# Kernel optimization log

Hardware: AMD Instinct MI355X
Metric: run time of the kernel (lower is better)

## Reference

```python
import jax, jax.numpy as jnp
import numpy as np

N_NODES = 50000
N_EDGES = 800000
NEG_SLOPE = 0.2


def _gat_layer(x, src, dst, W, al, ar, n_nodes):
    """Single multi-head GAT conv (DGL-style). Returns [N, H, D]."""
    H, D = al.shape
    feat = (x @ W).reshape(n_nodes, H, D)              # [N,H,D]
    el = jnp.einsum('nhd,hd->nh', feat, al)            # [N,H]
    er = jnp.einsum('nhd,hd->nh', feat, ar)            # [N,H]
    e = jax.nn.leaky_relu(el[src] + er[dst], NEG_SLOPE)  # [E,H]
    # numerically-stable edge softmax over incoming edges per dst node
    emax = jax.ops.segment_max(e, dst, num_segments=n_nodes)  # [N,H]
    emax = jnp.where(jnp.isfinite(emax), emax, 0.0)
    ee = jnp.exp(e - emax[dst])                        # [E,H]
    denom = jax.ops.segment_sum(ee, dst, num_segments=n_nodes)  # [N,H]
    alpha = ee / (denom[dst] + 1e-9)                   # [E,H]
    msg = alpha[:, :, None] * feat[src]                # [E,H,D]
    return jax.ops.segment_sum(msg, dst, num_segments=n_nodes)  # [N,H,D]


def setup_inputs() -> dict:
    key = jax.random.key(0)
    ks = jax.random.split(key, 9)
    features = jax.random.normal(ks[0], (N_NODES, 512), jnp.float32)
    src = jax.random.randint(ks[1], (N_EDGES,), 0, N_NODES)
    dst = jax.random.randint(ks[2], (N_EDGES,), 0, N_NODES)
    W1 = jax.random.normal(ks[3], (512, 256), jnp.float32) * 0.05
    al1 = jax.random.normal(ks[4], (8, 32), jnp.float32) * 0.05
    ar1 = jax.random.normal(ks[5], (8, 32), jnp.float32) * 0.05
    W2 = jax.random.normal(ks[6], (256, 320), jnp.float32) * 0.05
    al2 = jax.random.normal(ks[7], (8, 40), jnp.float32) * 0.05
    ar2 = jax.random.normal(ks[8], (8, 40), jnp.float32) * 0.05
    return {"features": features, "src": src, "dst": dst,
            "W1": W1, "al1": al1, "ar1": ar1,
            "W2": W2, "al2": al2, "ar2": ar2}


def reference(features, src, dst, W1, al1, ar1, W2, al2, ar2):
    n = features.shape[0]
    h = _gat_layer(features, src, dst, W1, al1, ar1, n)   # [N,8,32]
    h = jax.nn.elu(h.reshape(n, -1))                      # flatten(1) + ELU -> [N,256]
    h = _gat_layer(h, src, dst, W2, al2, ar2, n)          # [N,8,40]
    return h.mean(axis=1)                                 # head mean -> [N,40]
```

## Files before the change

### kernel.cpp

```cpp
#include <hip/hip_runtime.h>
#include <math.h>

typedef float f32x4 __attribute__((ext_vector_type(4)));
typedef __bf16 bf16x2 __attribute__((ext_vector_type(2)));
typedef __bf16 bf16x4 __attribute__((ext_vector_type(4)));
typedef __bf16 bf16x8 __attribute__((ext_vector_type(8)));


__global__ void hist_kernel(const int* __restrict__ dst, int* __restrict__ cnt, int E) {
    int e = blockIdx.x * blockDim.x + threadIdx.x;
    if (e < E) atomicAdd(&cnt[dst[e]], 1);
}

__global__ __launch_bounds__(256) void scan_blk(const int* __restrict__ cnt,
                                                int* __restrict__ incl,
                                                int* __restrict__ bsum, int n) {
    __shared__ int sd[256];
    const int t = threadIdx.x;
    int i = blockIdx.x * 256 + t;
    int v = (i < n) ? cnt[i] : 0;
    sd[t] = v;
    __syncthreads();
#pragma unroll
    for (int off = 1; off < 256; off <<= 1) {
        int x = (t >= off) ? sd[t - off] : 0;
        __syncthreads();
        sd[t] += x;
        __syncthreads();
    }
    if (i < n) incl[i] = sd[t];
    if (t == 255) bsum[blockIdx.x] = sd[255];
}

__global__ __launch_bounds__(256) void scan_top(const int* __restrict__ bsum,
                                                int* __restrict__ boff, int nb) {
    __shared__ int sd[256];
    const int t = threadIdx.x;
    int v = (t < nb) ? bsum[t] : 0;
    sd[t] = v;
    __syncthreads();
#pragma unroll
    for (int off = 1; off < 256; off <<= 1) {
        int x = (t >= off) ? sd[t - off] : 0;
        __syncthreads();
        sd[t] += x;
        __syncthreads();
    }
    if (t < nb) boff[t] = sd[t] - v;
}

__global__ void scan_fix(const int* __restrict__ incl, const int* __restrict__ boff,
                         const int* __restrict__ cnt, int* __restrict__ row_ptr,
                         int* __restrict__ cursor, int n) {
    int i = blockIdx.x * blockDim.x + threadIdx.x;
    if (i >= n) return;
    int total = incl[i] + boff[i >> 8];
    row_ptr[i + 1] = total;
    cursor[i] = total - cnt[i];
    if (i == 0) row_ptr[0] = 0;
}

__global__ void fill_kernel(const int* __restrict__ src, const int* __restrict__ dst,
                            int* __restrict__ cursor, int* __restrict__ ssrc,
                            int* __restrict__ sdst, int E) {
    int e = blockIdx.x * blockDim.x + threadIdx.x;
    if (e < E) {
        int d = dst[e];
        int pos = atomicAdd(&cursor[d], 1);
        ssrc[pos] = src[e];
        sdst[pos] = d;
    }
}

__global__ void pack_b_kernel(const float* __restrict__ W, __bf16* __restrict__ Bh,
                              __bf16* __restrict__ Bl, int K, int N) {
    int idx = blockIdx.x * blockDim.x + threadIdx.x;
    if (idx >= K * N) return;
    int e = idx & 7;
    int l = (idx >> 3) & 63;
    int c = idx >> 9;
    int ng = N >> 4;
    int g = c % ng;
    int k0 = (c / ng) << 5;
    int col = g * 16 + (l & 15);
    int k = k0 + ((l >> 4) << 3) + e;
    float x = W[(size_t)k * N + col];
    __bf16 h = (__bf16)x;
    Bh[idx] = h;
    Bl[idx] = (__bf16)(x - (float)h);
}

template <int BN, int NREP, bool FP32A>
__global__ __launch_bounds__(128) void gemm_fused(
    const float* __restrict__ Af, const __bf16* __restrict__ Ahg,
    const __bf16* __restrict__ Alg, const __bf16* __restrict__ Bph,
    const __bf16* __restrict__ Bpl, const float* __restrict__ al,
    const float* __restrict__ ar, __bf16* __restrict__ featb,
    float* __restrict__ el, float* __restrict__ er, int M, int K) {
    constexpr int WN = NREP * 16;
    constexpr int D = BN / 8;

    __shared__ __align__(16) __bf16 Ah[2][32][40];
    __shared__ __align__(16) __bf16 Al[2][32][40];
    __shared__ __align__(16) float ctile[2][16][WN + 1];

    const int t = threadIdx.x;
    const int lane = t & 63;
    const int wid = t >> 6;
    const int row0 = blockIdx.x * 32;
    const int colw = wid * WN;
    const int fr = lane & 15;
    const int kq = lane >> 4;
    const int kg = kq * 8;
    const int sr = t >> 2;
    const int sc = (t & 3) * 8;

    float4 av0, av1;
    bf16x8 avh, avl;

    auto loadA = [&](int k0) {
        int gr = row0 + sr;
        if (gr >= M) gr = M - 1;
        if constexpr (FP32A) {
            av0 = *(const float4*)&Af[(size_t)gr * K + k0 + sc];
            av1 = *(const float4*)&Af[(size_t)gr * K + k0 + sc + 4];
        } else {
            avh = *(const bf16x8*)&Ahg[(size_t)gr * K + k0 + sc];
            avl = *(const bf16x8*)&Alg[(size_t)gr * K + k0 + sc];
        }
    };
    auto storeA = [&](int p) {
        if constexpr (FP32A) {
            __bf16 h0 = (__bf16)av0.x, h1 = (__bf16)av0.y, h2 = (__bf16)av0.z,
                   h3 = (__bf16)av0.w;
            __bf16 h4 = (__bf16)av1.x, h5 = (__bf16)av1.y, h6 = (__bf16)av1.z,
                   h7 = (__bf16)av1.w;
            bf16x8 hv = {h0, h1, h2, h3, h4, h5, h6, h7};
            bf16x8 lv = {(__bf16)(av0.x - (float)h0), (__bf16)(av0.y - (float)h1),
                         (__bf16)(av0.z - (float)h2), (__bf16)(av0.w - (float)h3),
                         (__bf16)(av1.x - (float)h4), (__bf16)(av1.y - (float)h5),
                         (__bf16)(av1.z - (float)h6), (__bf16)(av1.w - (float)h7)};
            *(bf16x8*)&Ah[p][sr][sc] = hv;
            *(bf16x8*)&Al[p][sr][sc] = lv;
        } else {
            *(bf16x8*)&Ah[p][sr][sc] = avh;
            *(bf16x8*)&Al[p][sr][sc] = avl;
        }
    };

    f32x4 acc[2][NREP] = {};

    loadA(0);
    int p = 0;
    for (int k0 = 0; k0 < K; k0 += 32) {
        storeA(p);
        if (k0 + 32 < K) loadA(k0 + 32);
        bf16x8 bh[NREP], bl[NREP];
        const int c0 = (k0 >> 5) * (BN >> 4) + (colw >> 4);
#pragma unroll
        for (int n = 0; n < NREP; ++n) {
            size_t o = (size_t)(c0 + n) * 512 + lane * 8;
            bh[n] = *(const bf16x8*)&Bph[o];
            bl[n] = *(const bf16x8*)&Bpl[o];
        }
        __syncthreads();
        bf16x8 ah0 = *(const bf16x8*)&Ah[p][fr][kg];
        bf16x8 ah1 = *(const bf16x8*)&Ah[p][fr + 16][kg];
        bf16x8 al0 = *(const bf16x8*)&Al[p][fr][kg];
        bf16x8 al1 = *(const bf16x8*)&Al[p][fr + 16][kg];
#pragma unroll
        for (int n = 0; n < NREP; ++n) {
            acc[0][n] = __builtin_amdgcn_mfma_f32_16x16x32_bf16(ah0, bh[n], acc[0][n], 0, 0, 0);
            acc[0][n] = __builtin_amdgcn_mfma_f32_16x16x32_bf16(al0, bh[n], acc[0][n], 0, 0, 0);
            acc[0][n] = __builtin_amdgcn_mfma_f32_16x16x32_bf16(ah0, bl[n], acc[0][n], 0, 0, 0);
            acc[1][n] = __builtin_amdgcn_mfma_f32_16x16x32_bf16(ah1, bh[n], acc[1][n], 0, 0, 0);
            acc[1][n] = __builtin_amdgcn_mfma_f32_16x16x32_bf16(al1, bh[n], acc[1][n], 0, 0, 0);
            acc[1][n] = __builtin_amdgcn_mfma_f32_16x16x32_bf16(ah1, bl[n], acc[1][n], 0, 0, 0);
        }
        p ^= 1;
    }

#pragma unroll
    for (int m = 0; m < 2; ++m) {
        int rbase = row0 + m * 16 + kq * 4;
#pragma unroll
        for (int n = 0; n < NREP; ++n) {
            int col = colw + n * 16 + fr;
#pragma unroll
            for (int i = 0; i < 4; ++i) {
                int r = rbase + i;
                if (r < M) featb[(size_t)r * BN + col] = (__bf16)acc[m][n][i];
            }
        }
    }

#pragma unroll
    for (int m = 0; m < 2; ++m) {
#pragma unroll
        for (int n = 0; n < NREP; ++n)
#pragma unroll
            for (int i = 0; i < 4; ++i)
                ctile[wid][kq * 4 + i][n * 16 + fr] = acc[m][n][i];
        int r = lane & 15;
        int hh = lane >> 4;
        int h = wid * 4 + hh;
        float sl = 0.f, sr_ = 0.f;
#pragma unroll 8
        for (int d = 0; d < D; ++d) {
            float v = ctile[wid][r][hh * D + d];
            sl += v * al[h * D + d];
            sr_ += v * ar[h * D + d];
        }
        int gr = row0 + m * 16 + r;
        if (gr < M) {
            el[(size_t)gr * 8 + h] = sl;
            er[(size_t)gr * 8 + h] = sr_;
        }
        __syncthreads();
    }
}

__device__ __forceinline__ float leaky02(float x) { return x > 0.f ? x : 0.2f * x; }

__global__ void edge_score_kernel(const int* __restrict__ ssrc, const int* __restrict__ sdst,
                                  const float* __restrict__ el, const float* __restrict__ er,
                                  float* __restrict__ pe, int E) {
    int pos = blockIdx.x * blockDim.x + threadIdx.x;
    if (pos >= E) return;
    int s = ssrc[pos], d = sdst[pos];
    float4 l0 = *(const float4*)&el[(size_t)s * 8];
    float4 l1 = *(const float4*)&el[(size_t)s * 8 + 4];
    float4 r0 = *(const float4*)&er[(size_t)d * 8];
    float4 r1 = *(const float4*)&er[(size_t)d * 8 + 4];
    float4 o0 = {leaky02(l0.x + r0.x), leaky02(l0.y + r0.y),
                 leaky02(l0.z + r0.z), leaky02(l0.w + r0.w)};
    float4 o1 = {leaky02(l1.x + r1.x), leaky02(l1.y + r1.y),
                 leaky02(l1.z + r1.z), leaky02(l1.w + r1.w)};
    *(float4*)&pe[(size_t)pos * 8] = o0;
    *(float4*)&pe[(size_t)pos * 8 + 4] = o1;
}

template <int D, int MODE>
__global__ __launch_bounds__(256) void gat_aggregate(
    const __bf16* __restrict__ featb, const float* __restrict__ pe,
    const int* __restrict__ row_ptr, const int* __restrict__ ssrc,
    __bf16* __restrict__ outh, __bf16* __restrict__ outl,
    float* __restrict__ outf, int N) {
    constexpr int HD = 8 * D;
    constexpr int TAIL = HD - 256;
    __shared__ float red[4][MODE ? HD : 1];

    const int wid = threadIdx.x >> 6;
    const int lane = threadIdx.x & 63;
    const int n = blockIdx.x * 4 + wid;
    if (n >= N) return;

    const int beg = row_ptr[n];
    const int end = row_ptr[n + 1];
    const int hl = lane & 7;
    const int sl = lane >> 3;

    float m_l = -INFINITY;
    for (int idx = beg + sl; idx < end; idx += 8)
        m_l = fmaxf(m_l, pe[(size_t)idx * 8 + hl]);
    m_l = fmaxf(m_l, __shfl_xor(m_l, 8));
    m_l = fmaxf(m_l, __shfl_xor(m_l, 16));
    m_l = fmaxf(m_l, __shfl_xor(m_l, 32));
    float s_l = 0.f;
    for (int idx = beg + sl; idx < end; idx += 8)
        s_l += __expf(pe[(size_t)idx * 8 + hl] - m_l);
    s_l += __shfl_xor(s_l, 8);
    s_l += __shfl_xor(s_l, 16);
    s_l += __shfl_xor(s_l, 32);
    const float si_l = 1.0f / (s_l + 1e-9f);

    int hg[2], ht = 0;
#pragma unroll
    for (int g = 0; g < 2; ++g) hg[g] = (128 * g + 2 * lane) / D;
    if (TAIL) ht = (256 + lane) / D;

    float acc[2][2] = {};
    float acct = 0.f;
    int idx = beg;
    for (; idx + 4 <= end; idx += 4) {
        int ss[4];
        float aa[4];
#pragma unroll
        for (int uu = 0; uu < 4; ++uu) ss[uu] = ssrc[idx + uu];
#pragma unroll
        for (int uu = 0; uu < 4; ++uu)
            aa[uu] = __expf(pe[(size_t)(idx + uu) * 8 + hl] - m_l) * si_l;
        bf16x2 p[4][2];
        __bf16 pt[4];
#pragma unroll
        for (int uu = 0; uu < 4; ++uu) {
            const __bf16* f = featb + (size_t)ss[uu] * HD;
            p[uu][0] = *(const bf16x2*)&f[2 * lane];
            p[uu][1] = *(const bf16x2*)&f[128 + 2 * lane];
            if (TAIL) pt[uu] = f[256 + lane];
        }
#pragma unroll
        for (int uu = 0; uu < 4; ++uu) {
            float w0 = __shfl(aa[uu], hg[0]);
            float w1 = __shfl(aa[uu], hg[1]);
            acc[0][0] += w0 * (float)p[uu][0].x;
            acc[0][1] += w0 * (float)p[uu][0].y;
            acc[1][0] += w1 * (float)p[uu][1].x;
            acc[1][1] += w1 * (float)p[uu][1].y;
            if (TAIL) {
                float wt = __shfl(aa[uu], ht);
                acct += wt * (float)pt[uu];
            }
        }
    }
    for (; idx < end; ++idx) {
        int s = ssrc[idx];
        float a = __expf(pe[(size_t)idx * 8 + hl] - m_l) * si_l;
        const __bf16* f = featb + (size_t)s * HD;
        float w0 = __shfl(a, hg[0]);
        float w1 = __shfl(a, hg[1]);
        bf16x2 p0 = *(const bf16x2*)&f[2 * lane];
        bf16x2 p1 = *(const bf16x2*)&f[128 + 2 * lane];
        acc[0][0] += w0 * (float)p0.x;
        acc[0][1] += w0 * (float)p0.y;
        acc[1][0] += w1 * (float)p1.x;
        acc[1][1] += w1 * (float)p1.y;
        if (TAIL) {
            float wt = __shfl(a, ht);
            acct += wt * (float)f[256 + lane];
        }
    }

    if (MODE == 0) {
#pragma unroll
        for (int g = 0; g < 2; ++g) {
            float x0 = acc[g][0], x1 = acc[g][1];
            x0 = x0 > 0.f ? x0 : expm1f(x0);
            x1 = x1 > 0.f ? x1 : expm1f(x1);
            __bf16 h0 = (__bf16)x0, h1 = (__bf16)x1;
            bf16x2 vh = {h0, h1};
            bf16x2 vl = {(__bf16)(x0 - (float)h0), (__bf16)(x1 - (float)h1)};
            *(bf16x2*)&outh[(size_t)n * 256 + 128 * g + 2 * lane] = vh;
            *(bf16x2*)&outl[(size_t)n * 256 + 128 * g + 2 * lane] = vl;
        }
    } else {
#pragma unroll
        for (int g = 0; g < 2; ++g) {
            red[wid][128 * g + 2 * lane] = acc[g][0];
            red[wid][128 * g + 2 * lane + 1] = acc[g][1];
        }
        red[wid][256 + lane] = acct;
        if (lane < D) {
            float s = 0.f;
#pragma unroll
            for (int hh = 0; hh < 8; ++hh) s += red[wid][hh * D + lane];
            outf[(size_t)n * D + lane] = s * 0.125f;
        }
    }
}


extern "C" void kernel_launch(void* const* d_in, const int* in_sizes, int n_in,
                              void* d_out, int out_size, void* d_ws, size_t ws_size,
                              hipStream_t stream) {
    const float* features = (const float*)d_in[0];
    const int* src = (const int*)d_in[1];
    const int* dst = (const int*)d_in[2];
    const float* W1 = (const float*)d_in[3];
    const float* al1 = (const float*)d_in[4];
    const float* ar1 = (const float*)d_in[5];
    const float* W2 = (const float*)d_in[6];
    const float* al2 = (const float*)d_in[7];
    const float* ar2 = (const float*)d_in[8];

    const int N = in_sizes[0] / 512;
    const int E = in_sizes[1];

    char* ws = (char*)d_ws;
    size_t off = 0;
    auto alloc = [&](size_t bytes) -> void* {
        void* p = ws + off;
        off = (off + bytes + 255) & ~(size_t)255;
        return p;
    };
    __bf16* feat1b = (__bf16*)alloc((size_t)N * 256 * 2);
    __bf16* h_hi = (__bf16*)alloc((size_t)N * 256 * 2);
    __bf16* h_lo = (__bf16*)alloc((size_t)N * 256 * 2);
    __bf16* feat2b = (__bf16*)alloc((size_t)N * 320 * 2);
    float* pe = (float*)alloc((size_t)E * 8 * 4);
    float* el1 = (float*)alloc((size_t)N * 8 * 4);
    float* er1 = (float*)alloc((size_t)N * 8 * 4);
    float* el2 = (float*)alloc((size_t)N * 8 * 4);
    float* er2 = (float*)alloc((size_t)N * 8 * 4);
    int* cnt = (int*)alloc((size_t)N * 4);
    int* incl = (int*)alloc((size_t)N * 4);
    int* row_ptr = (int*)alloc((size_t)(N + 1) * 4);
    int* cursor = (int*)alloc((size_t)N * 4);
    int* bsum = (int*)alloc(256 * 4);
    int* boff = (int*)alloc(256 * 4);
    int* ssrc = (int*)alloc((size_t)E * 4);
    int* sdst = (int*)alloc((size_t)E * 4);
    __bf16* Bp1h = (__bf16*)alloc((size_t)512 * 256 * 2);
    __bf16* Bp1l = (__bf16*)alloc((size_t)512 * 256 * 2);
    __bf16* Bp2h = (__bf16*)alloc((size_t)256 * 320 * 2);
    __bf16* Bp2l = (__bf16*)alloc((size_t)256 * 320 * 2);

    const int NB = (N + 255) / 256;

    hipMemsetAsync(cnt, 0, (size_t)N * 4, stream);
    hist_kernel<<<(E + 255) / 256, 256, 0, stream>>>(dst, cnt, E);
    scan_blk<<<NB, 256, 0, stream>>>(cnt, incl, bsum, N);
    scan_top<<<1, 256, 0, stream>>>(bsum, boff, NB);
    scan_fix<<<NB, 256, 0, stream>>>(incl, boff, cnt, row_ptr, cursor, N);
    fill_kernel<<<(E + 255) / 256, 256, 0, stream>>>(src, dst, cursor, ssrc, sdst, E);

    pack_b_kernel<<<(512 * 256 + 255) / 256, 256, 0, stream>>>(W1, Bp1h, Bp1l, 512, 256);
    pack_b_kernel<<<(256 * 320 + 255) / 256, 256, 0, stream>>>(W2, Bp2h, Bp2l, 256, 320);

    const int mblk = (N + 31) / 32;

    gemm_fused<256, 8, true><<<mblk, 128, 0, stream>>>(
        features, nullptr, nullptr, Bp1h, Bp1l, al1, ar1, feat1b, el1, er1, N, 512);
    edge_score_kernel<<<(E + 255) / 256, 256, 0, stream>>>(ssrc, sdst, el1, er1, pe, E);
    gat_aggregate<32, 0><<<(N + 3) / 4, 256, 0, stream>>>(
        feat1b, pe, row_ptr, ssrc, h_hi, h_lo, nullptr, N);

    gemm_fused<320, 10, false><<<mblk, 128, 0, stream>>>(
        nullptr, h_hi, h_lo, Bp2h, Bp2l, al2, ar2, feat2b, el2, er2, N, 256);
    edge_score_kernel<<<(E + 255) / 256, 256, 0, stream>>>(ssrc, sdst, el2, er2, pe, E);
    gat_aggregate<40, 1><<<(N + 3) / 4, 256, 0, stream>>>(
        feat2b, pe, row_ptr, ssrc, nullptr, nullptr, (float*)d_out, N);
}
```

Measured before the change: 377.5 us.

## Use four waves per GEMM block with swizzled LDS A-tiles and union scratch

The fused GEMM now runs 256 threads (four waves) per block. Each wave covers half as many output columns, so it holds half as many accumulator and B registers, and launch bounds request higher occupancy. The A tile is stored in LDS in an MFMA-fragment-ready layout with an XOR swizzle, and it shares storage through a union with the epilogue ctile. The B global loads are now issued before the A store. The goal is more concurrent waves to hide global latency and fewer LDS bank conflicts. The cost is that each A load is now narrower (4 elements per thread), an extra barrier is added, and half the lanes sit idle in the el/er epilogue.

```diff
diff --git a/kernel.cpp b/kernel.cpp
--- a/kernel.cpp
+++ b/kernel.cpp
@@ -90,8 +90,10 @@
     Bl[idx] = (__bf16)(x - (float)h);
 }
 
+__device__ __forceinline__ int swz6(int x) { return x ^ (x >> 3); }
+
 template <int BN, int NREP, bool FP32A>
-__global__ __launch_bounds__(128) void gemm_fused(
+__global__ __launch_bounds__(256, 4) void gemm_fused(
     const float* __restrict__ Af, const __bf16* __restrict__ Ahg,
     const __bf16* __restrict__ Alg, const __bf16* __restrict__ Bph,
     const __bf16* __restrict__ Bpl, const float* __restrict__ al,
@@ -100,9 +102,15 @@
     constexpr int WN = NREP * 16;
     constexpr int D = BN / 8;
 
-    __shared__ __align__(16) __bf16 Ah[2][32][40];
-    __shared__ __align__(16) __bf16 Al[2][32][40];
-    __shared__ __align__(16) float ctile[2][16][WN + 1];
+    struct StageT {
+        __bf16 Ah[2][2][64][8];
+        __bf16 Al[2][2][64][8];
+    };
+    union Smem {
+        StageT s;
+        float ctile[4][16][WN + 1];
+    };
+    __shared__ __align__(16) Smem u;
 
     const int t = threadIdx.x;
     const int lane = t & 63;
@@ -111,40 +119,37 @@
     const int colw = wid * WN;
     const int fr = lane & 15;
     const int kq = lane >> 4;
-    const int kg = kq * 8;
-    const int sr = t >> 2;
-    const int sc = (t & 3) * 8;
-
-    float4 av0, av1;
-    bf16x8 avh, avl;
+    const int sr = t >> 3;
+    const int kc = (t & 7) * 4;
+    const int m_s = sr >> 4;
+    const int xs = (sr & 15) + 16 * (kc >> 3);
+    const int e0 = kc & 7;
+
+    float4 av;
+    bf16x4 avh, avl;
 
     auto loadA = [&](int k0) {
         int gr = row0 + sr;
         if (gr >= M) gr = M - 1;
         if constexpr (FP32A) {
-            av0 = *(const float4*)&Af[(size_t)gr * K + k0 + sc];
-            av1 = *(const float4*)&Af[(size_t)gr * K + k0 + sc + 4];
+            av = *(const float4*)&Af[(size_t)gr * K + k0 + kc];
         } else {
-            avh = *(const bf16x8*)&Ahg[(size_t)gr * K + k0 + sc];
-            avl = *(const bf16x8*)&Alg[(size_t)gr * K + k0 + sc];
+            avh = *(const bf16x4*)&Ahg[(size_t)gr * K + k0 + kc];
+            avl = *(const bf16x4*)&Alg[(size_t)gr * K + k0 + kc];
         }
     };
     auto storeA = [&](int p) {
         if constexpr (FP32A) {
-            __bf16 h0 = (__bf16)av0.x, h1 = (__bf16)av0.y, h2 = (__bf16)av0.z,
-                   h3 = (__bf16)av0.w;
-            __bf16 h4 = (__bf16)av1.x, h5 = (__bf16)av1.y, h6 = (__bf16)av1.z,
-                   h7 = (__bf16)av1.w;
-            bf16x8 hv = {h0, h1, h2, h3, h4, h5, h6, h7};
-            bf16x8 lv = {(__bf16)(av0.x - (float)h0), (__bf16)(av0.y - (float)h1),
-                         (__bf16)(av0.z - (float)h2), (__bf16)(av0.w - (float)h3),
-                         (__bf16)(av1.x - (float)h4), (__bf16)(av1.y - (float)h5),
-                         (__bf16)(av1.z - (float)h6), (__bf16)(av1.w - (float)h7)};
-            *(bf16x8*)&Ah[p][sr][sc] = hv;
-            *(bf16x8*)&Al[p][sr][sc] = lv;
+            __bf16 h0 = (__bf16)av.x, h1 = (__bf16)av.y, h2 = (__bf16)av.z,
+                   h3 = (__bf16)av.w;
+            bf16x4 hv = {h0, h1, h2, h3};
+            bf16x4 lv = {(__bf16)(av.x - (float)h0), (__bf16)(av.y - (float)h1),
+                         (__bf16)(av.z - (float)h2), (__bf16)(av.w - (float)h3)};
+            *(bf16x4*)&u.s.Ah[p][m_s][swz6(xs)][e0] = hv;
+            *(bf16x4*)&u.s.Al[p][m_s][swz6(xs)][e0] = lv;
         } else {
-            *(bf16x8*)&Ah[p][sr][sc] = avh;
-            *(bf16x8*)&Al[p][sr][sc] = avl;
+            *(bf16x4*)&u.s.Ah[p][m_s][swz6(xs)][e0] = avh;
+            *(bf16x4*)&u.s.Al[p][m_s][swz6(xs)][e0] = avl;
         }
     };
 
@@ -153,21 +158,22 @@
     loadA(0);
     int p = 0;
     for (int k0 = 0; k0 < K; k0 += 32) {
-        storeA(p);
-        if (k0 + 32 < K) loadA(k0 + 32);
         bf16x8 bh[NREP], bl[NREP];
-        const int c0 = (k0 >> 5) * (BN >> 4) + (colw >> 4);
+        const int c0 = (k0 >> 5) * (BN >> 4) + wid * NREP;
 #pragma unroll
         for (int n = 0; n < NREP; ++n) {
             size_t o = (size_t)(c0 + n) * 512 + lane * 8;
             bh[n] = *(const bf16x8*)&Bph[o];
             bl[n] = *(const bf16x8*)&Bpl[o];
         }
+        storeA(p);
+        if (k0 + 32 < K) loadA(k0 + 32);
         __syncthreads();
-        bf16x8 ah0 = *(const bf16x8*)&Ah[p][fr][kg];
-        bf16x8 ah1 = *(const bf16x8*)&Ah[p][fr + 16][kg];
-        bf16x8 al0 = *(const bf16x8*)&Al[p][fr][kg];
-        bf16x8 al1 = *(const bf16x8*)&Al[p][fr + 16][kg];
+        const int sl_ = swz6(lane);
+        bf16x8 ah0 = *(const bf16x8*)&u.s.Ah[p][0][sl_][0];
+        bf16x8 ah1 = *(const bf16x8*)&u.s.Ah[p][1][sl_][0];
+        bf16x8 al0 = *(const bf16x8*)&u.s.Al[p][0][sl_][0];
+        bf16x8 al1 = *(const bf16x8*)&u.s.Al[p][1][sl_][0];
 #pragma unroll
         for (int n = 0; n < NREP; ++n) {
             acc[0][n] = __builtin_amdgcn_mfma_f32_16x16x32_bf16(ah0, bh[n], acc[0][n], 0, 0, 0);
@@ -194,29 +200,31 @@
         }
     }
 
+    __syncthreads();
 #pragma unroll
     for (int m = 0; m < 2; ++m) {
 #pragma unroll
         for (int n = 0; n < NREP; ++n)
 #pragma unroll
             for (int i = 0; i < 4; ++i)
-                ctile[wid][kq * 4 + i][n * 16 + fr] = acc[m][n][i];
-        int r = lane & 15;
-        int hh = lane >> 4;
-        int h = wid * 4 + hh;
-        float sl = 0.f, sr_ = 0.f;
+                u.ctile[wid][kq * 4 + i][n * 16 + fr] = acc[m][n][i];
+        if (lane < 32) {
+            int r = lane & 15;
+            int hh = lane >> 4;
+            int h = wid * 2 + hh;
+            float sl = 0.f, sr_ = 0.f;
 #pragma unroll 8
-        for (int d = 0; d < D; ++d) {
-            float v = ctile[wid][r][hh * D + d];
-            sl += v * al[h * D + d];
-            sr_ += v * ar[h * D + d];
-        }
-        int gr = row0 + m * 16 + r;
-        if (gr < M) {
-            el[(size_t)gr * 8 + h] = sl;
-            er[(size_t)gr * 8 + h] = sr_;
-        }
-        __syncthreads();
+            for (int d = 0; d < D; ++d) {
+                float v = u.ctile[wid][r][hh * D + d];
+                sl += v * al[h * D + d];
+                sr_ += v * ar[h * D + d];
+            }
+            int gr = row0 + m * 16 + r;
+            if (gr < M) {
+                el[(size_t)gr * 8 + h] = sl;
+                er[(size_t)gr * 8 + h] = sr_;
+            }
+        }
     }
 }
 
@@ -419,13 +427,13 @@
 
     const int mblk = (N + 31) / 32;
 
-    gemm_fused<256, 8, true><<<mblk, 128, 0, stream>>>(
+    gemm_fused<256, 4, true><<<mblk, 256, 0, stream>>>(
         features, nullptr, nullptr, Bp1h, Bp1l, al1, ar1, feat1b, el1, er1, N, 512);
     edge_score_kernel<<<(E + 255) / 256, 256, 0, stream>>>(ssrc, sdst, el1, er1, pe, E);
     gat_aggregate<32, 0><<<(N + 3) / 4, 256, 0, stream>>>(
         feat1b, pe, row_ptr, ssrc, h_hi, h_lo, nullptr, N);
 
-    gemm_fused<320, 10, false><<<mblk, 128, 0, stream>>>(
+    gemm_fused<320, 5, false><<<mblk, 256, 0, stream>>>(
         nullptr, h_hi, h_lo, Bp2h, Bp2l, al2, ar2, feat2b, el2, er2, N, 256);
     edge_score_kernel<<<(E + 255) / 256, 256, 0, stream>>>(ssrc, sdst, el2, er2, pe, E);
     gat_aggregate<40, 1><<<(N + 3) / 4, 256, 0, stream>>>(
```

New measurement: 370.9 us. Within noise of the previous version (-1.7%).

## Restructure fused GEMM to 64-row tiles with direct global A-fragment loads

Applied to the files above, without the earlier changes.

The fused GEMM+attention-logit kernel now uses 256-thread blocks covering 64 rows, with four waves splitting the output columns. Each wave loads its A fragments straight from global memory into registers, converting to bf16 hi/lo, which removes the LDS double-buffer and its per-step barrier. K becomes a template parameter so the K loop fully unrolls, and the el/er epilogue is remapped to two heads per wave without a block barrier. The aim is better reuse of B per block and fewer syncs. The cost is that every wave redundantly fetches the same A rows through the cache, and register pressure is higher.

```diff
diff --git a/kernel.cpp b/kernel.cpp
--- a/kernel.cpp
+++ b/kernel.cpp
@@ -90,71 +90,38 @@
     Bl[idx] = (__bf16)(x - (float)h);
 }
 
-template <int BN, int NREP, bool FP32A>
-__global__ __launch_bounds__(128) void gemm_fused(
+template <int BN, int NREP, bool FP32A, int K>
+__global__ __launch_bounds__(256, 2) void gemm_fused(
     const float* __restrict__ Af, const __bf16* __restrict__ Ahg,
     const __bf16* __restrict__ Alg, const __bf16* __restrict__ Bph,
     const __bf16* __restrict__ Bpl, const float* __restrict__ al,
     const float* __restrict__ ar, __bf16* __restrict__ featb,
-    float* __restrict__ el, float* __restrict__ er, int M, int K) {
+    float* __restrict__ el, float* __restrict__ er, int M) {
     constexpr int WN = NREP * 16;
     constexpr int D = BN / 8;
 
-    __shared__ __align__(16) __bf16 Ah[2][32][40];
-    __shared__ __align__(16) __bf16 Al[2][32][40];
-    __shared__ __align__(16) float ctile[2][16][WN + 1];
+    __shared__ __align__(16) float ctile[4][16][WN + 1];
 
     const int t = threadIdx.x;
     const int lane = t & 63;
     const int wid = t >> 6;
-    const int row0 = blockIdx.x * 32;
+    const int row0 = blockIdx.x * 64;
     const int colw = wid * WN;
     const int fr = lane & 15;
     const int kq = lane >> 4;
     const int kg = kq * 8;
-    const int sr = t >> 2;
-    const int sc = (t & 3) * 8;
-
-    float4 av0, av1;
-    bf16x8 avh, avl;
-
-    auto loadA = [&](int k0) {
-        int gr = row0 + sr;
-        if (gr >= M) gr = M - 1;
-        if constexpr (FP32A) {
-            av0 = *(const float4*)&Af[(size_t)gr * K + k0 + sc];
-            av1 = *(const float4*)&Af[(size_t)gr * K + k0 + sc + 4];
-        } else {
-            avh = *(const bf16x8*)&Ahg[(size_t)gr * K + k0 + sc];
-            avl = *(const bf16x8*)&Alg[(size_t)gr * K + k0 + sc];
-        }
-    };
-    auto storeA = [&](int p) {
-        if constexpr (FP32A) {
-            __bf16 h0 = (__bf16)av0.x, h1 = (__bf16)av0.y, h2 = (__bf16)av0.z,
-                   h3 = (__bf16)av0.w;
-            __bf16 h4 = (__bf16)av1.x, h5 = (__bf16)av1.y, h6 = (__bf16)av1.z,
-                   h7 = (__bf16)av1.w;
-            bf16x8 hv = {h0, h1, h2, h3, h4, h5, h6, h7};
-            bf16x8 lv = {(__bf16)(av0.x - (float)h0), (__bf16)(av0.y - (float)h1),
-                         (__bf16)(av0.z - (float)h2), (__bf16)(av0.w - (float)h3),
-                         (__bf16)(av1.x - (float)h4), (__bf16)(av1.y - (float)h5),
-                         (__bf16)(av1.z - (float)h6), (__bf16)(av1.w - (float)h7)};
-            *(bf16x8*)&Ah[p][sr][sc] = hv;
-            *(bf16x8*)&Al[p][sr][sc] = lv;
-        } else {
-            *(bf16x8*)&Ah[p][sr][sc] = avh;
-            *(bf16x8*)&Al[p][sr][sc] = avl;
-        }
-    };
-
-    f32x4 acc[2][NREP] = {};
-
-    loadA(0);
-    int p = 0;
+
+    int ar_[4];
+#pragma unroll
+    for (int m = 0; m < 4; ++m) {
+        int gr = row0 + fr + m * 16;
+        ar_[m] = gr < M ? gr : M - 1;
+    }
+
+    f32x4 acc[4][NREP] = {};
+
+#pragma unroll
     for (int k0 = 0; k0 < K; k0 += 32) {
-        storeA(p);
-        if (k0 + 32 < K) loadA(k0 + 32);
         bf16x8 bh[NREP], bl[NREP];
         const int c0 = (k0 >> 5) * (BN >> 4) + (colw >> 4);
 #pragma unroll
@@ -163,25 +130,41 @@
             bh[n] = *(const bf16x8*)&Bph[o];
             bl[n] = *(const bf16x8*)&Bpl[o];
         }
-        __syncthreads();
-        bf16x8 ah0 = *(const bf16x8*)&Ah[p][fr][kg];
-        bf16x8 ah1 = *(const bf16x8*)&Ah[p][fr + 16][kg];
-        bf16x8 al0 = *(const bf16x8*)&Al[p][fr][kg];
-        bf16x8 al1 = *(const bf16x8*)&Al[p][fr + 16][kg];
-#pragma unroll
-        for (int n = 0; n < NREP; ++n) {
-            acc[0][n] = __builtin_amdgcn_mfma_f32_16x16x32_bf16(ah0, bh[n], acc[0][n], 0, 0, 0);
-            acc[0][n] = __builtin_amdgcn_mfma_f32_16x16x32_bf16(al0, bh[n], acc[0][n], 0, 0, 0);
-            acc[0][n] = __builtin_amdgcn_mfma_f32_16x16x32_bf16(ah0, bl[n], acc[0][n], 0, 0, 0);
-            acc[1][n] = __builtin_amdgcn_mfma_f32_16x16x32_bf16(ah1, bh[n], acc[1][n], 0, 0, 0);
-            acc[1][n] = __builtin_amdgcn_mfma_f32_16x16x32_bf16(al1, bh[n], acc[1][n], 0, 0, 0);
-            acc[1][n] = __builtin_amdgcn_mfma_f32_16x16x32_bf16(ah1, bl[n], acc[1][n], 0, 0, 0);
-        }
-        p ^= 1;
-    }
-
-#pragma unroll
-    for (int m = 0; m < 2; ++m) {
+        bf16x8 ah[4], alo[4];
+#pragma unroll
+        for (int m = 0; m < 4; ++m) {
+            if constexpr (FP32A) {
+                const float* p = &Af[(size_t)ar_[m] * K + k0 + kg];
+                float4 v0 = *(const float4*)p;
+                float4 v1 = *(const float4*)(p + 4);
+                __bf16 h0 = (__bf16)v0.x, h1 = (__bf16)v0.y, h2 = (__bf16)v0.z,
+                       h3 = (__bf16)v0.w;
+                __bf16 h4 = (__bf16)v1.x, h5 = (__bf16)v1.y, h6 = (__bf16)v1.z,
+                       h7 = (__bf16)v1.w;
+                bf16x8 hv = {h0, h1, h2, h3, h4, h5, h6, h7};
+                bf16x8 lv = {(__bf16)(v0.x - (float)h0), (__bf16)(v0.y - (float)h1),
+                             (__bf16)(v0.z - (float)h2), (__bf16)(v0.w - (float)h3),
+                             (__bf16)(v1.x - (float)h4), (__bf16)(v1.y - (float)h5),
+                             (__bf16)(v1.z - (float)h6), (__bf16)(v1.w - (float)h7)};
+                ah[m] = hv;
+                alo[m] = lv;
+            } else {
+                ah[m] = *(const bf16x8*)&Ahg[(size_t)ar_[m] * K + k0 + kg];
+                alo[m] = *(const bf16x8*)&Alg[(size_t)ar_[m] * K + k0 + kg];
+            }
+        }
+#pragma unroll
+        for (int m = 0; m < 4; ++m)
+#pragma unroll
+            for (int n = 0; n < NREP; ++n) {
+                acc[m][n] = __builtin_amdgcn_mfma_f32_16x16x32_bf16(ah[m], bh[n], acc[m][n], 0, 0, 0);
+                acc[m][n] = __builtin_amdgcn_mfma_f32_16x16x32_bf16(alo[m], bh[n], acc[m][n], 0, 0, 0);
+                acc[m][n] = __builtin_amdgcn_mfma_f32_16x16x32_bf16(ah[m], bl[n], acc[m][n], 0, 0, 0);
+            }
+    }
+
+#pragma unroll
+    for (int m = 0; m < 4; ++m) {
         int rbase = row0 + m * 16 + kq * 4;
 #pragma unroll
         for (int n = 0; n < NREP; ++n) {
@@ -195,28 +178,29 @@
     }
 
 #pragma unroll
-    for (int m = 0; m < 2; ++m) {
+    for (int m = 0; m < 4; ++m) {
 #pragma unroll
         for (int n = 0; n < NREP; ++n)
 #pragma unroll
             for (int i = 0; i < 4; ++i)
                 ctile[wid][kq * 4 + i][n * 16 + fr] = acc[m][n][i];
-        int r = lane & 15;
-        int hh = lane >> 4;
-        int h = wid * 4 + hh;
-        float sl = 0.f, sr_ = 0.f;
+        if (lane < 32) {
+            int r = lane & 15;
+            int hh = lane >> 4;
+            int h = wid * 2 + hh;
+            float sl = 0.f, sr_ = 0.f;
 #pragma unroll 8
-        for (int d = 0; d < D; ++d) {
-            float v = ctile[wid][r][hh * D + d];
-            sl += v * al[h * D + d];
-            sr_ += v * ar[h * D + d];
-        }
-        int gr = row0 + m * 16 + r;
-        if (gr < M) {
-            el[(size_t)gr * 8 + h] = sl;
-            er[(size_t)gr * 8 + h] = sr_;
-        }
-        __syncthreads();
+            for (int d = 0; d < D; ++d) {
+                float v = ctile[wid][r][hh * D + d];
+                sl += v * al[h * D + d];
+                sr_ += v * ar[h * D + d];
+            }
+            int gr = row0 + m * 16 + r;
+            if (gr < M) {
+                el[(size_t)gr * 8 + h] = sl;
+                er[(size_t)gr * 8 + h] = sr_;
+            }
+        }
     }
 }
 
@@ -417,16 +401,16 @@
     pack_b_kernel<<<(512 * 256 + 255) / 256, 256, 0, stream>>>(W1, Bp1h, Bp1l, 512, 256);
     pack_b_kernel<<<(256 * 320 + 255) / 256, 256, 0, stream>>>(W2, Bp2h, Bp2l, 256, 320);
 
-    const int mblk = (N + 31) / 32;
-
-    gemm_fused<256, 8, true><<<mblk, 128, 0, stream>>>(
-        features, nullptr, nullptr, Bp1h, Bp1l, al1, ar1, feat1b, el1, er1, N, 512);
+    const int mblk = (N + 63) / 64;
+
+    gemm_fused<256, 4, true, 512><<<mblk, 256, 0, stream>>>(
+        features, nullptr, nullptr, Bp1h, Bp1l, al1, ar1, feat1b, el1, er1, N);
     edge_score_kernel<<<(E + 255) / 256, 256, 0, stream>>>(ssrc, sdst, el1, er1, pe, E);
     gat_aggregate<32, 0><<<(N + 3) / 4, 256, 0, stream>>>(
         feat1b, pe, row_ptr, ssrc, h_hi, h_lo, nullptr, N);
 
-    gemm_fused<320, 10, false><<<mblk, 128, 0, stream>>>(
-        nullptr, h_hi, h_lo, Bp2h, Bp2l, al2, ar2, feat2b, el2, er2, N, 256);
+    gemm_fused<320, 5, false, 256><<<mblk, 256, 0, stream>>>(
+        nullptr, h_hi, h_lo, Bp2h, Bp2l, al2, ar2, feat2b, el2, er2, N);
     edge_score_kernel<<<(E + 255) / 256, 256, 0, stream>>>(ssrc, sdst, el2, er2, pe, E);
     gat_aggregate<40, 1><<<(N + 3) / 4, 256, 0, stream>>>(
         feat2b, pe, row_ptr, ssrc, nullptr, nullptr, (float*)d_out, N);
```

New measurement: 435.0 us. 15.2% more time.
